# Kernel tuning notes

Hardware: AMD Instinct MI355X
Metric: run time of the kernel (lower is better)

## Reference

```python
import jax, jax.numpy as jnp
import numpy as np

GAMMA0 = 1.0


def patch_to_image(patches):
    # patches: [b, n_patch, patch_dim, 1, T] -> image [b, 1, g*p, g*p, T]
    b, n_patch, patch_dim, _, T = patches.shape
    p = int(patch_dim ** 0.5)
    g = int(n_patch ** 0.5)
    img = patches[:, :, :, 0, :]                      # [b, n_patch, p*p, T]
    img = jnp.transpose(img, (0, 3, 1, 2))            # [b, T, n_patch, p*p]
    img = img.reshape(b, T, g, g, p, p)
    img = jnp.transpose(img, (0, 1, 2, 4, 3, 5)).reshape(b, T, 1, g * p, g * p)
    return jnp.transpose(img, (0, 2, 3, 4, 1))        # [b, 1, g*p, g*p, T]


def setup_inputs() -> dict:
    key = jax.random.key(0)
    k0, k1, k2, k3, k4, k5 = jax.random.split(key, 6)
    X = jax.random.normal(k0, (32, 64, 300, 1, 50), dtype=jnp.float32)
    U = jax.random.normal(k1, (32, 1, 40, 1, 50), dtype=jnp.float32)
    x0 = jax.random.normal(k2, (32, 64, 300, 1), dtype=jnp.float32)
    # dictionaries, column-normalized like torch's norm(dim=2, keepdim=True)
    A = jax.random.uniform(k3, (300, 300), dtype=jnp.float32)
    A = A / jnp.linalg.norm(A, axis=0, keepdims=True)
    B = jax.random.uniform(k4, (300, 40), dtype=jnp.float32)
    B = B / jnp.linalg.norm(B, axis=0, keepdims=True)
    C = jax.random.uniform(k5, (256, 300), dtype=jnp.float32)
    C = C / jnp.linalg.norm(C, axis=0, keepdims=True)
    return {"X": X, "U": U, "x0": x0, "A": A, "B": B, "C": C}


def reference(X, U, x0, A, B, C):
    # X: [b, P, 300, 1, T]  U: [b, 1, 40, 1, T]  x0: [b, P, 300, 1]
    # Prediction x_hat_t = A @ x_{t-1}, with x_{-1} = x0 (vectorized over T)
    x_prev = jnp.concatenate([x0[..., None], X[..., :-1]], axis=-1)   # [b,P,300,1,T]
    X_pred = jnp.einsum('ij,bpjut->bpiut', A, x_prev)                 # [b,P,300,1,T]
    # Reconstruction recon_t = C @ x_t, assembled into frames
    recon = jnp.einsum('dj,bpjut->bpdut', C, X)                       # [b,P,256,1,T]
    vid_recon = patch_to_image(recon)                                 # [b,1,128,128,T]
    # Cause state: gamma_t * sum_patches |x_t|
    Bu = jnp.einsum('ij,bqjut->bqiut', B, U)                          # [b,1,300,1,T]
    gamma = GAMMA0 * (1.0 + jnp.exp(-Bu)) / 2.0
    X_U = gamma * jnp.sum(jnp.abs(X), axis=1, keepdims=True)          # [b,1,300,1,T]
    return (vid_recon, X_pred, X_U)
```

## Files before the change

kernel.cpp:

```cpp
#include <hip/hip_runtime.h>

typedef _Float16 half8 __attribute__((ext_vector_type(8)));
typedef _Float16 half4v __attribute__((ext_vector_type(4)));
typedef float f32x4 __attribute__((ext_vector_type(4)));

#define OFF_PRED 26214400
#define OFF_XU   56934400

__global__ void build_M(const float* __restrict__ A, const float* __restrict__ C,
                        _Float16* __restrict__ M) {
    int idx = blockIdx.x * 256 + threadIdx.x;
    if (idx >= 640 * 320) return;
    int e    = idx & 7;
    int lane = (idx >> 3) & 63;
    int fs   = idx >> 9;
    int mt = fs / 10, ks = fs % 10;
    int m = mt * 16 + (lane & 15);
    int k = ks * 32 + (lane >> 4) * 8 + e;
    float v = 0.f;
    if (k < 300) {
        if (m < 256) v = C[m * 300 + k];
        else if (m < 556) v = A[(m - 256) * 300 + k];
    }
    M[idx] = (_Float16)v;
}

__global__ __launch_bounds__(256, 3) void gemm_main(
    const float* __restrict__ X, const float* __restrict__ x0,
    const _Float16* __restrict__ M, float* __restrict__ out)
{
    __shared__ _Float16 lds[64 * 320];
    char* ldsb = (char*)lds;
    const int bid = blockIdx.x;
    const int bp = bid >> 1, mhalf = bid & 1;
    const int b = bp >> 6, p = bp & 63;
    const int tid = threadIdx.x;
    const float* Xbp = X + bp * 15000;

    const int wave = tid >> 6, lane = tid & 63;
    const int lr = lane & 15, lg = lane >> 4;
    const int g = wave;

    #pragma unroll
    for (int u = 0; u < 20; u++)
        *(unsigned long long*)(ldsb + tid * 8 + u * 2048) = 0ULL;
    __syncthreads();

    if (tid < 75) {
        f32x4 v = *(const f32x4*)(x0 + bp * 300 + tid * 4);
        half4v h4 = { (_Float16)v.x, (_Float16)v.y, (_Float16)v.z, (_Float16)v.w };
        *(half4v*)(ldsb + tid * 8) = h4;
    }
    for (int i = tid; i < 3750; i += 256) {
        int t = i % 50, jq = i / 50;
        const float* s = Xbp + (jq * 4) * 50 + t;
        half4v h4 = { (_Float16)s[0], (_Float16)s[50], (_Float16)s[100], (_Float16)s[150] };
        int row = t + 1;
        *(half4v*)(ldsb + row * 640 + ((jq * 8) ^ ((row & 7) << 4))) = h4;
    }
    __syncthreads();

    f32x4 acc[5][4];
    #pragma unroll
    for (int j = 0; j < 5; j++)
        #pragma unroll
        for (int nt = 0; nt < 4; nt++)
            acc[j][nt] = (f32x4){0.f, 0.f, 0.f, 0.f};

    const _Float16* Mw = M + (mhalf * 4 + g) * 50 * 512 + lane * 8;
    #define LDSA(nt, ks) (*(const half8*)(ldsb + ((nt) * 16 + lr) * 640 + \
                         (((ks) * 64 + lg * 16) ^ ((lr & 7) << 4))))

    #pragma unroll
    for (int ks = 0; ks < 10; ks++) {
        half8 bf0 = *(const half8*)(Mw + (0 * 10 + ks) * 512);
        half8 bf1 = *(const half8*)(Mw + (1 * 10 + ks) * 512);
        half8 bf2 = *(const half8*)(Mw + (2 * 10 + ks) * 512);
        half8 bf3 = *(const half8*)(Mw + (3 * 10 + ks) * 512);
        half8 bf4 = *(const half8*)(Mw + (4 * 10 + ks) * 512);
        #pragma unroll
        for (int nt = 0; nt < 4; nt++) {
            half8 a = LDSA(nt, ks);
            acc[0][nt] = __builtin_amdgcn_mfma_f32_16x16x32_f16(a, bf0, acc[0][nt], 0, 0, 0);
            acc[1][nt] = __builtin_amdgcn_mfma_f32_16x16x32_f16(a, bf1, acc[1][nt], 0, 0, 0);
            acc[2][nt] = __builtin_amdgcn_mfma_f32_16x16x32_f16(a, bf2, acc[2][nt], 0, 0, 0);
            acc[3][nt] = __builtin_amdgcn_mfma_f32_16x16x32_f16(a, bf3, acc[3][nt], 0, 0, 0);
            acc[4][nt] = __builtin_amdgcn_mfma_f32_16x16x32_f16(a, bf4, acc[4][nt], 0, 0, 0);
        }
    }

    const int gr = p >> 3, gc = p & 7;
    #pragma unroll
    for (int j = 0; j < 5; j++) {
        int colm = mhalf * 320 + g * 80 + j * 16 + lr;
        if (colm < 256) {
            int base = b * 819200 + ((gr * 16 + (colm >> 4)) * 128 + gc * 16 + (colm & 15)) * 50;
            #pragma unroll
            for (int nt = 0; nt < 4; nt++) {
                int t0 = nt * 16 + lg * 4;
                if (t0 == 0) {
                    out[base + 0] = acc[j][0][1];
                    out[base + 1] = acc[j][0][2];
                    out[base + 2] = acc[j][0][3];
                } else if (t0 <= 46) {
                    f32x4 v = acc[j][nt];
                    __builtin_memcpy(&out[base + t0 - 1], &v, 16);
                } else if (t0 == 48) {
                    out[base + 47] = acc[j][nt][0];
                    out[base + 48] = acc[j][nt][1];
                    out[base + 49] = acc[j][nt][2];
                }
            }
        } else if (colm < 556) {
            int base = OFF_PRED + (bp * 300 + (colm - 256)) * 50;
            #pragma unroll
            for (int nt = 0; nt < 4; nt++) {
                int t0 = nt * 16 + lg * 4;
                if (t0 <= 46) {
                    f32x4 v = acc[j][nt];
                    __builtin_memcpy(&out[base + t0], &v, 16);
                } else if (t0 == 48) {
                    out[base + 48] = acc[j][nt][0];
                    out[base + 49] = acc[j][nt][1];
                }
            }
        }
    }
}

__global__ void xu_kernel(const float* __restrict__ X, const float* __restrict__ U,
                          const float* __restrict__ B, float* __restrict__ out) {
    int id = blockIdx.x * 256 + threadIdx.x;
    if (id >= 480000) return;
    int t = id % 50;
    int i = (id / 50) % 300;
    int b = id / 15000;
    const float* xp = X + b * 960000 + i * 50 + t;
    float s = 0.f;
    #pragma unroll 8
    for (int pp = 0; pp < 64; pp++) s += fabsf(xp[pp * 15000]);
    float bu = 0.f;
    const float* up = U + b * 2000 + t;
    const float* Bp = B + i * 40;
    #pragma unroll 8
    for (int q = 0; q < 40; q++) bu += Bp[q] * up[q * 50];
    out[OFF_XU + id] = 0.5f * (1.f + expf(-bu)) * s;
}

extern "C" void kernel_launch(void* const* d_in, const int* in_sizes, int n_in,
                              void* d_out, int out_size, void* d_ws, size_t ws_size,
                              hipStream_t stream) {
    const float* X  = (const float*)d_in[0];
    const float* U  = (const float*)d_in[1];
    const float* x0 = (const float*)d_in[2];
    const float* A  = (const float*)d_in[3];
    const float* B  = (const float*)d_in[4];
    const float* C  = (const float*)d_in[5];
    float* out = (float*)d_out;
    _Float16* M = (_Float16*)d_ws;

    build_M<<<800, 256, 0, stream>>>(A, C, M);
    gemm_main<<<4096, 256, 0, stream>>>(X, x0, M, out);
    xu_kernel<<<1875, 256, 0, stream>>>(X, U, B, out);
}
```

Measured before the change: 144.5 us.

## Make GEMM blocks loop over patches with double-buffered LDS prefetch

The GEMM becomes a persistent-style kernel: 256 blocks of 512 threads each handle 8 (batch, patch) tiles and compute all 640 M rows at once, instead of splitting M across two blocks. Each block loads X only once per tile, where before it was loaded twice. The next tile's X is read into registers while the current tile's outputs are stored, then written to the alternate LDS buffer. This trades occupancy (one large block per CU, more registers per thread) for less global read traffic and overlap of loads with stores.

```diff
diff --git a/kernel.cpp b/kernel.cpp
--- a/kernel.cpp
+++ b/kernel.cpp
@@ -6,6 +6,7 @@
 
 #define OFF_PRED 26214400
 #define OFF_XU   56934400
+#define NBP 8
 
 __global__ void build_M(const float* __restrict__ A, const float* __restrict__ C,
                         _Float16* __restrict__ M) {
@@ -25,107 +26,143 @@
     M[idx] = (_Float16)v;
 }
 
-__global__ __launch_bounds__(256, 3) void gemm_main(
+__global__ __launch_bounds__(512, 2) void gemm_main(
     const float* __restrict__ X, const float* __restrict__ x0,
     const _Float16* __restrict__ M, float* __restrict__ out)
 {
-    __shared__ _Float16 lds[64 * 320];
-    char* ldsb = (char*)lds;
-    const int bid = blockIdx.x;
-    const int bp = bid >> 1, mhalf = bid & 1;
-    const int b = bp >> 6, p = bp & 63;
+    __shared__ _Float16 lds[2][64 * 320];
     const int tid = threadIdx.x;
-    const float* Xbp = X + bp * 15000;
-
     const int wave = tid >> 6, lane = tid & 63;
     const int lr = lane & 15, lg = lane >> 4;
     const int g = wave;
-
+    const int bp0 = blockIdx.x * NBP;
+
+    int offg[8], offl[8];
     #pragma unroll
-    for (int u = 0; u < 20; u++)
-        *(unsigned long long*)(ldsb + tid * 8 + u * 2048) = 0ULL;
+    for (int u = 0; u < 8; u++) {
+        int i = tid + u * 512;
+        int t = i % 50, jq = i / 50;
+        offg[u] = jq * 200 + t;
+        int row = t + 1;
+        offl[u] = row * 640 + ((jq * 8) ^ ((row & 7) << 4));
+    }
+    const bool v7 = tid < 166;
+
+    const _Float16* Mw = M + g * 50 * 512 + lane * 8;
+
+    {
+        char* l0 = (char*)&lds[0][0];
+        #pragma unroll
+        for (int u = 0; u < 20; u++)
+            *(unsigned long long*)(l0 + tid * 8 + u * 4096) = 0ULL;
+    }
     __syncthreads();
 
-    if (tid < 75) {
-        f32x4 v = *(const f32x4*)(x0 + bp * 300 + tid * 4);
-        half4v h4 = { (_Float16)v.x, (_Float16)v.y, (_Float16)v.z, (_Float16)v.w };
-        *(half4v*)(ldsb + tid * 8) = h4;
-    }
-    for (int i = tid; i < 3750; i += 256) {
-        int t = i % 50, jq = i / 50;
-        const float* s = Xbp + (jq * 4) * 50 + t;
-        half4v h4 = { (_Float16)s[0], (_Float16)s[50], (_Float16)s[100], (_Float16)s[150] };
-        int row = t + 1;
-        *(half4v*)(ldsb + row * 640 + ((jq * 8) ^ ((row & 7) << 4))) = h4;
-    }
+    float sx[8][4], s0x[4];
+
+#define STAGE_L(bp) { const float* Xb_ = X + (bp) * 15000;                          \
+    _Pragma("unroll")                                                                \
+    for (int u = 0; u < 8; u++) if (u < 7 || v7) {                                   \
+        const float* s_ = Xb_ + offg[u];                                             \
+        sx[u][0] = s_[0]; sx[u][1] = s_[50]; sx[u][2] = s_[100]; sx[u][3] = s_[150]; \
+    }                                                                                \
+    if (tid < 75) { f32x4 v_ = *(const f32x4*)(x0 + (bp) * 300 + tid * 4);           \
+        s0x[0] = v_.x; s0x[1] = v_.y; s0x[2] = v_.z; s0x[3] = v_.w; } }
+
+#define STAGE_W(wbc) { char* wb_ = (wbc);                                            \
+    _Pragma("unroll")                                                                \
+    for (int u = 0; u < 8; u++) if (u < 7 || v7) {                                   \
+        half4v h4_ = {(_Float16)sx[u][0], (_Float16)sx[u][1],                        \
+                      (_Float16)sx[u][2], (_Float16)sx[u][3]};                       \
+        *(half4v*)(wb_ + offl[u]) = h4_;                                             \
+    }                                                                                \
+    if (tid < 75) { half4v h4_ = {(_Float16)s0x[0], (_Float16)s0x[1],                \
+                                  (_Float16)s0x[2], (_Float16)s0x[3]};               \
+        *(half4v*)(wb_ + tid * 8) = h4_; } }
+
+    STAGE_L(bp0);
+    STAGE_W((char*)&lds[0][0]);
     __syncthreads();
 
-    f32x4 acc[5][4];
-    #pragma unroll
-    for (int j = 0; j < 5; j++)
+    #define LDSA(base, nt, ks) (*(const half8*)((base) + ((nt) * 16 + lr) * 640 + \
+                               (((ks) * 64 + lg * 16) ^ ((lr & 7) << 4))))
+
+    for (int it = 0; it < NBP; ++it) {
+        const int bp = bp0 + it;
+        const int b = bp >> 6, p = bp & 63;
+        char* rb = (char*)&lds[it & 1][0];
+
+        f32x4 acc[5][4];
         #pragma unroll
-        for (int nt = 0; nt < 4; nt++)
-            acc[j][nt] = (f32x4){0.f, 0.f, 0.f, 0.f};
-
-    const _Float16* Mw = M + (mhalf * 4 + g) * 50 * 512 + lane * 8;
-    #define LDSA(nt, ks) (*(const half8*)(ldsb + ((nt) * 16 + lr) * 640 + \
-                         (((ks) * 64 + lg * 16) ^ ((lr & 7) << 4))))
-
-    #pragma unroll
-    for (int ks = 0; ks < 10; ks++) {
-        half8 bf0 = *(const half8*)(Mw + (0 * 10 + ks) * 512);
-        half8 bf1 = *(const half8*)(Mw + (1 * 10 + ks) * 512);
-        half8 bf2 = *(const half8*)(Mw + (2 * 10 + ks) * 512);
-        half8 bf3 = *(const half8*)(Mw + (3 * 10 + ks) * 512);
-        half8 bf4 = *(const half8*)(Mw + (4 * 10 + ks) * 512);
+        for (int j = 0; j < 5; j++)
+            #pragma unroll
+            for (int nt = 0; nt < 4; nt++)
+                acc[j][nt] = (f32x4){0.f, 0.f, 0.f, 0.f};
+
         #pragma unroll
-        for (int nt = 0; nt < 4; nt++) {
-            half8 a = LDSA(nt, ks);
-            acc[0][nt] = __builtin_amdgcn_mfma_f32_16x16x32_f16(a, bf0, acc[0][nt], 0, 0, 0);
-            acc[1][nt] = __builtin_amdgcn_mfma_f32_16x16x32_f16(a, bf1, acc[1][nt], 0, 0, 0);
-            acc[2][nt] = __builtin_amdgcn_mfma_f32_16x16x32_f16(a, bf2, acc[2][nt], 0, 0, 0);
-            acc[3][nt] = __builtin_amdgcn_mfma_f32_16x16x32_f16(a, bf3, acc[3][nt], 0, 0, 0);
-            acc[4][nt] = __builtin_amdgcn_mfma_f32_16x16x32_f16(a, bf4, acc[4][nt], 0, 0, 0);
-        }
-    }
-
-    const int gr = p >> 3, gc = p & 7;
-    #pragma unroll
-    for (int j = 0; j < 5; j++) {
-        int colm = mhalf * 320 + g * 80 + j * 16 + lr;
-        if (colm < 256) {
-            int base = b * 819200 + ((gr * 16 + (colm >> 4)) * 128 + gc * 16 + (colm & 15)) * 50;
+        for (int ks = 0; ks < 10; ks++) {
+            half8 bf0 = *(const half8*)(Mw + (0 * 10 + ks) * 512);
+            half8 bf1 = *(const half8*)(Mw + (1 * 10 + ks) * 512);
+            half8 bf2 = *(const half8*)(Mw + (2 * 10 + ks) * 512);
+            half8 bf3 = *(const half8*)(Mw + (3 * 10 + ks) * 512);
+            half8 bf4 = *(const half8*)(Mw + (4 * 10 + ks) * 512);
             #pragma unroll
             for (int nt = 0; nt < 4; nt++) {
-                int t0 = nt * 16 + lg * 4;
-                if (t0 == 0) {
-                    out[base + 0] = acc[j][0][1];
-                    out[base + 1] = acc[j][0][2];
-                    out[base + 2] = acc[j][0][3];
-                } else if (t0 <= 46) {
-                    f32x4 v = acc[j][nt];
-                    __builtin_memcpy(&out[base + t0 - 1], &v, 16);
-                } else if (t0 == 48) {
-                    out[base + 47] = acc[j][nt][0];
-                    out[base + 48] = acc[j][nt][1];
-                    out[base + 49] = acc[j][nt][2];
-                }
+                half8 a = LDSA(rb, nt, ks);
+                acc[0][nt] = __builtin_amdgcn_mfma_f32_16x16x32_f16(a, bf0, acc[0][nt], 0, 0, 0);
+                acc[1][nt] = __builtin_amdgcn_mfma_f32_16x16x32_f16(a, bf1, acc[1][nt], 0, 0, 0);
+                acc[2][nt] = __builtin_amdgcn_mfma_f32_16x16x32_f16(a, bf2, acc[2][nt], 0, 0, 0);
+                acc[3][nt] = __builtin_amdgcn_mfma_f32_16x16x32_f16(a, bf3, acc[3][nt], 0, 0, 0);
+                acc[4][nt] = __builtin_amdgcn_mfma_f32_16x16x32_f16(a, bf4, acc[4][nt], 0, 0, 0);
             }
-        } else if (colm < 556) {
-            int base = OFF_PRED + (bp * 300 + (colm - 256)) * 50;
+        }
+
+        if (it + 1 < NBP) STAGE_L(bp + 1);
+
+        {
+            const int gr = p >> 3, gc = p & 7;
             #pragma unroll
-            for (int nt = 0; nt < 4; nt++) {
-                int t0 = nt * 16 + lg * 4;
-                if (t0 <= 46) {
-                    f32x4 v = acc[j][nt];
-                    __builtin_memcpy(&out[base + t0], &v, 16);
-                } else if (t0 == 48) {
-                    out[base + 48] = acc[j][nt][0];
-                    out[base + 49] = acc[j][nt][1];
+            for (int j = 0; j < 5; j++) {
+                int colm = g * 80 + j * 16 + lr;
+                if (colm < 256) {
+                    int base = b * 819200 + ((gr * 16 + (colm >> 4)) * 128 + gc * 16 + (colm & 15)) * 50;
+                    #pragma unroll
+                    for (int nt = 0; nt < 4; nt++) {
+                        int t0 = nt * 16 + lg * 4;
+                        if (t0 == 0) {
+                            out[base + 0] = acc[j][0][1];
+                            out[base + 1] = acc[j][0][2];
+                            out[base + 2] = acc[j][0][3];
+                        } else if (t0 <= 46) {
+                            f32x4 v = acc[j][nt];
+                            __builtin_memcpy(&out[base + t0 - 1], &v, 16);
+                        } else if (t0 == 48) {
+                            out[base + 47] = acc[j][nt][0];
+                            out[base + 48] = acc[j][nt][1];
+                            out[base + 49] = acc[j][nt][2];
+                        }
+                    }
+                } else if (colm < 556) {
+                    int base = OFF_PRED + (bp * 300 + (colm - 256)) * 50;
+                    #pragma unroll
+                    for (int nt = 0; nt < 4; nt++) {
+                        int t0 = nt * 16 + lg * 4;
+                        if (t0 <= 46) {
+                            f32x4 v = acc[j][nt];
+                            __builtin_memcpy(&out[base + t0], &v, 16);
+                        } else if (t0 == 48) {
+                            out[base + 48] = acc[j][nt][0];
+                            out[base + 49] = acc[j][nt][1];
+                        }
+                    }
                 }
             }
         }
-    }
+
+        if (it + 1 < NBP) STAGE_W((char*)&lds[(it & 1) ^ 1][0]);
+        __syncthreads();
+    }
+    #undef LDSA
 }
 
 __global__ void xu_kernel(const float* __restrict__ X, const float* __restrict__ U,
@@ -160,6 +197,6 @@
     _Float16* M = (_Float16*)d_ws;
 
     build_M<<<800, 256, 0, stream>>>(A, C, M);
-    gemm_main<<<4096, 256, 0, stream>>>(X, x0, M, out);
+    gemm_main<<<256, 512, 0, stream>>>(X, x0, M, out);
     xu_kernel<<<1875, 256, 0, stream>>>(X, U, B, out);
 }
```

After: 325.7 us. 125% more time.
